# Kernel tuning notes

Hardware: AMD Instinct MI355X
Metric: run time of the kernel (lower is better)

## Reference

```python
import jax, jax.numpy as jnp
import numpy as np


def setup_inputs() -> dict:
    key = jax.random.key(0)
    k1, k2, k3 = jax.random.split(key, 3)
    N, M, D = 4096, 4096, 256
    x = jax.random.normal(k1, (N, D), dtype=jnp.float32)
    y = jax.random.normal(k2, (M, D), dtype=jnp.float32)
    # torch init: normal(0.0, 0.1)
    log_band_width = 0.1 * jax.random.normal(k3, (D,), dtype=jnp.float32)
    return {"x": x, "y": y, "log_band_width": log_band_width}


def reference(x, y, log_band_width):
    # ARD kernel: k(x,y) = exp(-0.5 * sum_d (x_d - y_d)^2 / bw_d), bw = exp(log_bw)
    # Quadratic expansion to avoid the O(N*M*D) broadcast intermediate:
    # scale inputs by 1/sqrt(bw), then sqdist = |xw|^2 + |yw|^2 - 2 xw @ yw^T
    inv_sqrt_bw = jnp.exp(-0.5 * log_band_width)  # [D]
    xw = x * inv_sqrt_bw  # [N, D]
    yw = y * inv_sqrt_bw  # [M, D]
    x2 = jnp.sum(xw * xw, axis=-1)  # [N]
    y2 = jnp.sum(yw * yw, axis=-1)  # [M]
    cross = xw @ yw.T  # [N, M] GEMM
    pdist = x2[:, None] + y2[None, :] - 2.0 * cross
    pdist = jnp.maximum(pdist, 0.0)  # clamp tiny negatives from fp cancellation
    return jnp.exp(-0.5 * pdist)
```

## Files before the change

### kernel.cpp

```cpp
#include <hip/hip_runtime.h>
#include <hip/hip_bf16.h>


typedef __attribute__((ext_vector_type(8))) short bf16x8;
typedef __attribute__((ext_vector_type(4))) float f32x4;

#define NN 4096
#define MM 4096
#define DD 256

#define BM 128
#define BN 128

#define GLOAD16(gp, lp)                                                        \
    __builtin_amdgcn_global_load_lds(                                          \
        (const __attribute__((address_space(1))) void*)(gp),                   \
        (__attribute__((address_space(3))) void*)(lp), 16, 0, 0)

__global__ __launch_bounds__(256) void ard_prep(
    const float* __restrict__ x, const float* __restrict__ y,
    const float* __restrict__ lbw,
    __hip_bfloat16* __restrict__ xw, __hip_bfloat16* __restrict__ yw,
    float* __restrict__ x2, float* __restrict__ y2)
{
    const int lane = threadIdx.x & 63;
    const int row  = blockIdx.x * 4 + (threadIdx.x >> 6);

    const float* src;
    __hip_bfloat16* dst;
    float* nrm;
    if (row < NN) {
        src = x + (size_t)row * DD;
        dst = xw + (size_t)row * DD;
        nrm = x2 + row;
    } else {
        const int r = row - NN;
        src = y + (size_t)r * DD;
        dst = yw + (size_t)r * DD;
        nrm = y2 + r;
    }

    const float4 v  = reinterpret_cast<const float4*>(src)[lane];
    const float4 lw = reinterpret_cast<const float4*>(lbw)[lane];

    float wv[4];
    wv[0] = v.x * __expf(-0.5f * lw.x);
    wv[1] = v.y * __expf(-0.5f * lw.y);
    wv[2] = v.z * __expf(-0.5f * lw.z);
    wv[3] = v.w * __expf(-0.5f * lw.w);

    __hip_bfloat16 h[4];
    float s = 0.0f;
#pragma unroll
    for (int j = 0; j < 4; ++j) {
        h[j] = __float2bfloat16(wv[j]);
        const float f = __bfloat162float(h[j]);
        s += f * f;
    }

    reinterpret_cast<uint2*>(dst)[lane] = *reinterpret_cast<uint2*>(h);

#pragma unroll
    for (int off = 32; off > 0; off >>= 1) s += __shfl_down(s, off);
    if (lane == 0) *nrm = s;
}

__global__ __launch_bounds__(256) void ard_gemm(
    const __hip_bfloat16* __restrict__ A,
    const __hip_bfloat16* __restrict__ B,
    const float* __restrict__ x2, const float* __restrict__ y2,
    float* __restrict__ out)
{
    __shared__ __align__(16) __hip_bfloat16 sA[BM * DD];
    __shared__ __align__(16) __hip_bfloat16 sB[BN * DD];

    const int tid  = threadIdx.x;
    const int lane = tid & 63;
    const int wid  = tid >> 6;
    const int wr   = wid >> 1;
    const int wc   = wid & 1;

    const int bi = blockIdx.y;
    const int bj = blockIdx.x;
    const size_t arow0 = (size_t)bi * BM;
    const size_t brow0 = (size_t)bj * BN;

    const int srow = lane >> 5;
    const int slot = lane & 31;

#pragma unroll
    for (int t = 0; t < 16; ++t) {
        const int r    = wid * 32 + t * 2;
        const int row  = r + srow;
        const int lcb  = (slot * 16) ^ ((row & 7) << 4);
        GLOAD16((const char*)(A + (arow0 + row) * DD) + lcb, (char*)sA + r * 512);
        GLOAD16((const char*)(B + (brow0 + row) * DD) + lcb, (char*)sB + r * 512);
    }
    __syncthreads();

    f32x4 acc[4][4] = {};
    const int frow = lane & 15;
    const int fkb  = (lane >> 4) * 16;
    const int aswz = (frow & 7) << 4;

#pragma unroll
    for (int kk = 0; kk < 8; ++kk) {
        bf16x8 a[4], b[4];
        const int kb = kk * 64;
#pragma unroll
        for (int m = 0; m < 4; ++m) {
            const int row = wr * 64 + m * 16 + frow;
            a[m] = *reinterpret_cast<const bf16x8*>(
                (const char*)sA + row * 512 + ((kb + fkb) ^ aswz));
        }
#pragma unroll
        for (int n = 0; n < 4; ++n) {
            const int row = wc * 64 + n * 16 + frow;
            b[n] = *reinterpret_cast<const bf16x8*>(
                (const char*)sB + row * 512 + ((kb + fkb) ^ aswz));
        }
#pragma unroll
        for (int m = 0; m < 4; ++m)
#pragma unroll
            for (int n = 0; n < 4; ++n)
                acc[m][n] = __builtin_amdgcn_mfma_f32_16x16x32_bf16(
                    a[m], b[n], acc[m][n], 0, 0, 0);
    }

    const int row0 = bi * BM + wr * 64;
    const int col0 = bj * BN + wc * 64;
    const int cl   = lane & 15;
    const int rsub = (lane >> 4) * 4;

#pragma unroll
    for (int m = 0; m < 4; ++m) {
        const int rbase = row0 + m * 16 + rsub;
        float xv[4];
#pragma unroll
        for (int j = 0; j < 4; ++j) xv[j] = x2[rbase + j];
#pragma unroll
        for (int n = 0; n < 4; ++n) {
            const int c  = col0 + n * 16 + cl;
            const float yv = y2[c];
#pragma unroll
            for (int j = 0; j < 4; ++j) {
                float t = xv[j] + yv - 2.0f * acc[m][n][j];
                t = fmaxf(t, 0.0f);
                out[(size_t)(rbase + j) * MM + c] = __expf(-0.5f * t);
            }
        }
    }
}

extern "C" void kernel_launch(void* const* d_in, const int* in_sizes, int n_in,
                              void* d_out, int out_size, void* d_ws, size_t ws_size,
                              hipStream_t stream) {
    const float* x   = (const float*)d_in[0];
    const float* y   = (const float*)d_in[1];
    const float* lbw = (const float*)d_in[2];
    float* out = (float*)d_out;

    char* ws = (char*)d_ws;
    __hip_bfloat16* xw = (__hip_bfloat16*)ws;
    __hip_bfloat16* yw = (__hip_bfloat16*)(ws + (size_t)2 * 1024 * 1024);
    float* x2 = (float*)(ws + (size_t)4 * 1024 * 1024);
    float* y2 = (float*)(ws + (size_t)4 * 1024 * 1024 + 16384);

    ard_prep<<<(NN + MM) / 4, 256, 0, stream>>>(x, y, lbw, xw, yw, x2, y2);

    dim3 grid(MM / BN, NN / BM);
    ard_gemm<<<grid, 256, 0, stream>>>(xw, yw, x2, y2, out);
}
```

Baseline: 33.43 us.

## Split K into two staged halves, double wave count, vectorize nontemporal epilogue stores

```diff
diff --git a/kernel.cpp b/kernel.cpp
--- a/kernel.cpp
+++ b/kernel.cpp
@@ -11,6 +11,7 @@
 
 #define BM 128
 #define BN 128
+#define HK 128
 
 #define GLOAD16(gp, lp)                                                        \
     __builtin_amdgcn_global_load_lds(                                          \
@@ -65,89 +66,100 @@
     if (lane == 0) *nrm = s;
 }
 
-__global__ __launch_bounds__(256) void ard_gemm(
+__global__ __launch_bounds__(512) void ard_gemm(
     const __hip_bfloat16* __restrict__ A,
     const __hip_bfloat16* __restrict__ B,
     const float* __restrict__ x2, const float* __restrict__ y2,
     float* __restrict__ out)
 {
-    __shared__ __align__(16) __hip_bfloat16 sA[BM * DD];
-    __shared__ __align__(16) __hip_bfloat16 sB[BN * DD];
+    __shared__ __align__(16) __hip_bfloat16 sA[2][BM * HK];
+    __shared__ __align__(16) __hip_bfloat16 sB[2][BN * HK];
 
     const int tid  = threadIdx.x;
     const int lane = tid & 63;
     const int wid  = tid >> 6;
-    const int wr   = wid >> 1;
-    const int wc   = wid & 1;
+    const int wr   = wid >> 2;
+    const int wc   = wid & 3;
 
     const int bi = blockIdx.y;
     const int bj = blockIdx.x;
     const size_t arow0 = (size_t)bi * BM;
     const size_t brow0 = (size_t)bj * BN;
 
-    const int srow = lane >> 5;
-    const int slot = lane & 31;
+    const int crow = lane >> 4;
+    const int slot = lane & 15;
+
+    auto stage = [&](int h) {
+        const int colb = h * 256;
+#pragma unroll
+        for (int t = 0; t < 4; ++t) {
+            const int r   = wid * 16 + t * 4;
+            const int row = r + crow;
+            const int lcb = colb + ((slot * 16) ^ ((row & 7) << 4));
+            GLOAD16((const char*)(A + (arow0 + row) * DD) + lcb,
+                    (char*)&sA[h][0] + r * 256);
+            GLOAD16((const char*)(B + (brow0 + row) * DD) + lcb,
+                    (char*)&sB[h][0] + r * 256);
+        }
+    };
+
+    f32x4 acc[4][2] = {};
+    const int frow = lane & 15;
+    const int fkb  = (lane >> 4) * 16;
+    const int swz  = (frow & 7) << 4;
+
+    stage(0);
+    __syncthreads();
+    stage(1);
 
 #pragma unroll
-    for (int t = 0; t < 16; ++t) {
-        const int r    = wid * 32 + t * 2;
-        const int row  = r + srow;
-        const int lcb  = (slot * 16) ^ ((row & 7) << 4);
-        GLOAD16((const char*)(A + (arow0 + row) * DD) + lcb, (char*)sA + r * 512);
-        GLOAD16((const char*)(B + (brow0 + row) * DD) + lcb, (char*)sB + r * 512);
-    }
-    __syncthreads();
-
-    f32x4 acc[4][4] = {};
-    const int frow = lane & 15;
-    const int fkb  = (lane >> 4) * 16;
-    const int aswz = (frow & 7) << 4;
-
+    for (int h = 0; h < 2; ++h) {
+        if (h == 1) __syncthreads();
 #pragma unroll
-    for (int kk = 0; kk < 8; ++kk) {
-        bf16x8 a[4], b[4];
-        const int kb = kk * 64;
+        for (int kk = 0; kk < 4; ++kk) {
+            const int kb = kk * 64 + fkb;
+            bf16x8 a[4], b[2];
 #pragma unroll
-        for (int m = 0; m < 4; ++m) {
-            const int row = wr * 64 + m * 16 + frow;
-            a[m] = *reinterpret_cast<const bf16x8*>(
-                (const char*)sA + row * 512 + ((kb + fkb) ^ aswz));
+            for (int m = 0; m < 4; ++m) {
+                const int row = wr * 64 + m * 16 + frow;
+                a[m] = *reinterpret_cast<const bf16x8*>(
+                    (const char*)&sA[h][0] + row * 256 + (kb ^ swz));
+            }
+#pragma unroll
+            for (int n = 0; n < 2; ++n) {
+                const int row = wc * 32 + n * 16 + frow;
+                b[n] = *reinterpret_cast<const bf16x8*>(
+                    (const char*)&sB[h][0] + row * 256 + (kb ^ swz));
+            }
+#pragma unroll
+            for (int m = 0; m < 4; ++m)
+#pragma unroll
+                for (int n = 0; n < 2; ++n)
+                    acc[m][n] = __builtin_amdgcn_mfma_f32_16x16x32_bf16(
+                        b[n], a[m], acc[m][n], 0, 0, 0);
         }
-#pragma unroll
-        for (int n = 0; n < 4; ++n) {
-            const int row = wc * 64 + n * 16 + frow;
-            b[n] = *reinterpret_cast<const bf16x8*>(
-                (const char*)sB + row * 512 + ((kb + fkb) ^ aswz));
-        }
-#pragma unroll
-        for (int m = 0; m < 4; ++m)
-#pragma unroll
-            for (int n = 0; n < 4; ++n)
-                acc[m][n] = __builtin_amdgcn_mfma_f32_16x16x32_bf16(
-                    a[m], b[n], acc[m][n], 0, 0, 0);
     }
 
     const int row0 = bi * BM + wr * 64;
-    const int col0 = bj * BN + wc * 64;
+    const int col0 = bj * BN + wc * 32;
     const int cl   = lane & 15;
     const int rsub = (lane >> 4) * 4;
 
 #pragma unroll
     for (int m = 0; m < 4; ++m) {
-        const int rbase = row0 + m * 16 + rsub;
-        float xv[4];
+        const int r = row0 + m * 16 + cl;
+        const float xv = x2[r];
+        float* orow = out + (size_t)r * MM;
 #pragma unroll
-        for (int j = 0; j < 4; ++j) xv[j] = x2[rbase + j];
-#pragma unroll
-        for (int n = 0; n < 4; ++n) {
-            const int c  = col0 + n * 16 + cl;
-            const float yv = y2[c];
-#pragma unroll
-            for (int j = 0; j < 4; ++j) {
-                float t = xv[j] + yv - 2.0f * acc[m][n][j];
-                t = fmaxf(t, 0.0f);
-                out[(size_t)(rbase + j) * MM + c] = __expf(-0.5f * t);
-            }
+        for (int n = 0; n < 2; ++n) {
+            const int c = col0 + n * 16 + rsub;
+            const float4 yv = *reinterpret_cast<const float4*>(y2 + c);
+            f32x4 o;
+            o.x = __expf(-0.5f * fmaxf(xv + yv.x - 2.0f * acc[m][n][0], 0.0f));
+            o.y = __expf(-0.5f * fmaxf(xv + yv.y - 2.0f * acc[m][n][1], 0.0f));
+            o.z = __expf(-0.5f * fmaxf(xv + yv.z - 2.0f * acc[m][n][2], 0.0f));
+            o.w = __expf(-0.5f * fmaxf(xv + yv.w - 2.0f * acc[m][n][3], 0.0f));
+            __builtin_nontemporal_store(o, reinterpret_cast<f32x4*>(orow + c));
         }
     }
 }
@@ -169,5 +181,5 @@
     ard_prep<<<(NN + MM) / 4, 256, 0, stream>>>(x, y, lbw, xw, yw, x2, y2);
 
     dim3 grid(MM / BN, NN / BM);
-    ard_gemm<<<grid, 256, 0, stream>>>(xw, yw, x2, y2, out);
+    ard_gemm<<<grid, 512, 0, stream>>>(xw, yw, x2, y2, out);
 }
```

After: 35.83 us. +7.2%, slower.
